# Optimization experiments

Hardware: AMD Instinct MI355X
Metric: run time of the kernel (lower is better)

The kernel has to match this reference:

```python
import jax, jax.numpy as jnp
import numpy as np

IT = 3  # BP iterations
ROWS, N = 144, 576  # H dims: wman_N0576_R34 -> 144 checks, 576 vars
ROW_DEG = 6  # check-node degree


def _make_H():
    rng = np.random.default_rng(0)
    H = np.zeros((ROWS, N), np.float32)
    for i in range(ROWS):
        cols = rng.choice(N, size=ROW_DEG, replace=False)
        H[i, cols] = 1.0
    return jnp.asarray(H)


def _quantize(x, eta, qk):
    # 4-level soft quantization: softmax over -(x-qk)^2/(2 eta^2)
    logits = -(x[..., None] - qk) ** 2 / (2.0 * eta ** 2 + 1e-12)
    w = jax.nn.softmax(logits, axis=-1)
    return jnp.sum(w * qk, axis=-1)


def setup_inputs() -> dict:
    key = jax.random.key(0)
    k1, = jax.random.split(key, 1)
    batch = 512
    r = jax.random.normal(k1, (batch, N), dtype=jnp.float32)
    H = _make_H()
    alpha = jnp.ones((IT,), jnp.float32) * 0.7
    beta = jnp.ones((IT,), jnp.float32) * 0.05
    eta = jnp.ones((IT,), jnp.float32) * 0.7
    qk = jnp.linspace(-4.0, 4.0, 4).astype(jnp.float32)
    return {"r": r, "H": H, "alpha": alpha, "beta": beta, "eta": eta, "qk": qk}


def reference(r, H, alpha, beta, eta, qk):
    B, n = r.shape
    Hmask = H == 1
    node_idx = jnp.arange(n)[None, None, :]
    M = H[None] * r[:, None, :]          # (B, ROWS, N)
    E = jnp.zeros_like(M)
    for t in range(IT):
        # --- check-to-variable (min-sum with masked top-2) ---
        masked_abs = jnp.where(Hmask, jnp.abs(M), jnp.inf)
        neg_top, idx = jax.lax.top_k(-masked_abs, 2)  # two smallest
        min1 = -neg_top[..., 0:1]
        min2 = -neg_top[..., 1:2]
        idx1 = idx[..., 0:1]
        E_abs = jnp.where(node_idx == idx1, min2, min1)
        signs = jnp.sign(M)
        valid_signs = jnp.where(Hmask, signs, 1.0)
        row_sign_prod = jnp.prod(valid_signs, axis=2, keepdims=True)
        E_sign = row_sign_prod * valid_signs
        E = alpha[t] * E_sign * jnp.maximum(0.0, E_abs - beta[t])
        E = E * H
        E = _quantize(E, eta[t], qk)
        # --- variable-to-check update ---
        sum_E = jnp.sum(E, axis=1, keepdims=True)
        M = (r[:, None, :] + sum_E - E) * H[None]
        M = _quantize(M, eta[t], qk)
    return r + jnp.sum(E, axis=1)
```

## Files before the change

kernel.cpp:

```cpp
#include <hip/hip_runtime.h>
#include <math.h>

#define IT 3
#define ROWS 144
#define NCOLS 576
#define ROW_DEG 6

__device__ __forceinline__ float quantize4(float x, float inv2e,
                                           float q0, float q1, float q2, float q3) {
    float d0 = x - q0, d1 = x - q1, d2 = x - q2, d3 = x - q3;
    float l0 = -d0 * d0 * inv2e;
    float l1 = -d1 * d1 * inv2e;
    float l2 = -d2 * d2 * inv2e;
    float l3 = -d3 * d3 * inv2e;
    float mx = fmaxf(fmaxf(l0, l1), fmaxf(l2, l3));
    float w0 = __expf(l0 - mx), w1 = __expf(l1 - mx);
    float w2 = __expf(l2 - mx), w3 = __expf(l3 - mx);
    float s = w0 + w1 + w2 + w3;
    return (w0 * q0 + w1 * q1 + w2 * q2 + w3 * q3) / s;
}

__device__ __forceinline__ float signf(float x) {
    return (x > 0.0f) ? 1.0f : ((x < 0.0f) ? -1.0f : 0.0f);
}

__global__ __launch_bounds__(64) void extract_cols_kernel(
    const float* __restrict__ H, int* __restrict__ cols)
{
    const int row  = blockIdx.x;
    const int lane = threadIdx.x;
    int base = 0;
    for (int i = 0; i < NCOLS / 64; ++i) {
        int col = i * 64 + lane;
        bool nz = H[row * NCOLS + col] != 0.0f;
        unsigned long long mask = __ballot(nz);
        if (nz) {
            int rank = base + __popcll(mask & ((1ull << lane) - 1ull));
            if (rank < ROW_DEG) cols[row * ROW_DEG + rank] = col;
        }
        base += __popcll(mask);
    }
}

__global__ __launch_bounds__(192) void decode_kernel(
    const float* __restrict__ r, const int* __restrict__ cols,
    const float* __restrict__ alpha, const float* __restrict__ beta,
    const float* __restrict__ eta, const float* __restrict__ qk,
    float* __restrict__ out)
{
    __shared__ float s_r[NCOLS];
    __shared__ float s_sumE[NCOLS];

    const int b = blockIdx.x;
    const float* rb = r + (size_t)b * NCOLS;
    for (int j = threadIdx.x; j < NCOLS; j += blockDim.x) s_r[j] = rb[j];

    const float q0 = qk[0], q1 = qk[1], q2 = qk[2], q3 = qk[3];
    float al[IT], be[IT], i2e[IT];
    for (int t = 0; t < IT; ++t) {
        al[t] = alpha[t];
        be[t] = beta[t];
        float et = eta[t];
        i2e[t] = 1.0f / (2.0f * et * et + 1e-12f);
    }

    const int row = threadIdx.x;
    const bool active = row < ROWS;

    int   c[ROW_DEG];
    float m[ROW_DEG];
    float E[ROW_DEG];

    __syncthreads();
    if (active) {
        for (int e = 0; e < ROW_DEG; ++e) {
            c[e] = cols[row * ROW_DEG + e];
            m[e] = s_r[c[e]];
        }
    }

    for (int t = 0; t < IT; ++t) {
        const float inv2e = i2e[t];

        __syncthreads();
        for (int j = threadIdx.x; j < NCOLS; j += blockDim.x) s_sumE[j] = 0.0f;
        __syncthreads();

        if (active) {
            float min1 = INFINITY, min2 = INFINITY;
            int idx = -1;
            float sp = 1.0f;
            for (int e = 0; e < ROW_DEG; ++e) {
                float a = fabsf(m[e]);
                sp *= signf(m[e]);
                if (a < min1) { min2 = min1; min1 = a; idx = e; }
                else if (a < min2) { min2 = a; }
            }
            for (int e = 0; e < ROW_DEG; ++e) {
                float eabs = (e == idx) ? min2 : min1;
                float v = al[t] * sp * signf(m[e]) * fmaxf(0.0f, eabs - be[t]);
                v = quantize4(v, inv2e, q0, q1, q2, q3);
                E[e] = v;
                atomicAdd(&s_sumE[c[e]], v);
            }
        }
        __syncthreads();

        if (t < IT - 1 && active) {
            for (int e = 0; e < ROW_DEG; ++e) {
                float v = s_r[c[e]] + s_sumE[c[e]] - E[e];
                m[e] = quantize4(v, inv2e, q0, q1, q2, q3);
            }
        }
    }

    float* ob = out + (size_t)b * NCOLS;
    for (int j = threadIdx.x; j < NCOLS; j += blockDim.x) ob[j] = s_r[j] + s_sumE[j];
}

extern "C" void kernel_launch(void* const* d_in, const int* in_sizes, int n_in,
                              void* d_out, int out_size, void* d_ws, size_t ws_size,
                              hipStream_t stream) {
    const float* r     = (const float*)d_in[0];
    const float* H     = (const float*)d_in[1];
    const float* alpha = (const float*)d_in[2];
    const float* beta  = (const float*)d_in[3];
    const float* eta   = (const float*)d_in[4];
    const float* qk    = (const float*)d_in[5];
    float* out = (float*)d_out;

    int* cols = (int*)d_ws;
    const int batch = in_sizes[0] / NCOLS;

    hipLaunchKernelGGL(extract_cols_kernel, dim3(ROWS), dim3(64), 0, stream,
                       H, cols);
    hipLaunchKernelGGL(decode_kernel, dim3(batch), dim3(192), 0, stream,
                       r, cols, alpha, beta, eta, qk, out);
}
```

Baseline: 80.72 us.

## Fuse column extraction into decoder and use single-exp quantizer

Removes the separate column-extraction kernel: each block now scans H itself and keeps the column indices in shared memory. The 4-level softmax quantizer is rewritten as one exp of a scaled input plus two cubic polynomials in that exponential, with precomputed per-iteration constants. This assumes the quantization levels are evenly spaced and clamps the exponent. Row/output copies are vectorized to float4. Every block now redundantly reads all of H, which adds L2 traffic in exchange for dropping one launch.

```diff
diff --git a/kernel.cpp b/kernel.cpp
--- a/kernel.cpp
+++ b/kernel.cpp
@@ -5,66 +5,77 @@
 #define ROWS 144
 #define NCOLS 576
 #define ROW_DEG 6
+#define NTHREADS 192
+#define NWAVES 3
 
-__device__ __forceinline__ float quantize4(float x, float inv2e,
-                                           float q0, float q1, float q2, float q3) {
-    float d0 = x - q0, d1 = x - q1, d2 = x - q2, d3 = x - q3;
-    float l0 = -d0 * d0 * inv2e;
-    float l1 = -d1 * d1 * inv2e;
-    float l2 = -d2 * d2 * inv2e;
-    float l3 = -d3 * d3 * inv2e;
-    float mx = fmaxf(fmaxf(l0, l1), fmaxf(l2, l3));
-    float w0 = __expf(l0 - mx), w1 = __expf(l1 - mx);
-    float w2 = __expf(l2 - mx), w3 = __expf(l3 - mx);
-    float s = w0 + w1 + w2 + w3;
-    return (w0 * q0 + w1 * q1 + w2 * q2 + w3 * q3) / s;
+__device__ __forceinline__ float quantize1(float x, float S,
+                                           float K0, float K1, float K2, float K3,
+                                           float KQ0, float KQ1, float KQ2, float KQ3) {
+    float s = fminf(fmaxf(x * S, -30.0f), 30.0f);
+    float B = __expf(s);
+    float den = ((K3 * B + K2) * B + K1) * B + K0;
+    float num = ((KQ3 * B + KQ2) * B + KQ1) * B + KQ0;
+    return num * __builtin_amdgcn_rcpf(den);
 }
 
 __device__ __forceinline__ float signf(float x) {
     return (x > 0.0f) ? 1.0f : ((x < 0.0f) ? -1.0f : 0.0f);
 }
 
-__global__ __launch_bounds__(64) void extract_cols_kernel(
-    const float* __restrict__ H, int* __restrict__ cols)
-{
-    const int row  = blockIdx.x;
-    const int lane = threadIdx.x;
-    int base = 0;
-    for (int i = 0; i < NCOLS / 64; ++i) {
-        int col = i * 64 + lane;
-        bool nz = H[row * NCOLS + col] != 0.0f;
-        unsigned long long mask = __ballot(nz);
-        if (nz) {
-            int rank = base + __popcll(mask & ((1ull << lane) - 1ull));
-            if (rank < ROW_DEG) cols[row * ROW_DEG + rank] = col;
-        }
-        base += __popcll(mask);
-    }
-}
-
-__global__ __launch_bounds__(192) void decode_kernel(
-    const float* __restrict__ r, const int* __restrict__ cols,
+__global__ __launch_bounds__(NTHREADS) void decode_kernel(
+    const float* __restrict__ r, const float* __restrict__ H,
     const float* __restrict__ alpha, const float* __restrict__ beta,
     const float* __restrict__ eta, const float* __restrict__ qk,
     float* __restrict__ out)
 {
-    __shared__ float s_r[NCOLS];
-    __shared__ float s_sumE[NCOLS];
+    __shared__ __align__(16) float s_r[NCOLS];
+    __shared__ __align__(16) float s_sumE[NCOLS];
+    __shared__ int s_cols[ROWS * ROW_DEG];
 
-    const int b = blockIdx.x;
-    const float* rb = r + (size_t)b * NCOLS;
-    for (int j = threadIdx.x; j < NCOLS; j += blockDim.x) s_r[j] = rb[j];
+    const int b   = blockIdx.x;
+    const int tid = threadIdx.x;
+
+    const float4* rb4 = reinterpret_cast<const float4*>(r + (size_t)b * NCOLS);
+    float4* s_r4 = reinterpret_cast<float4*>(s_r);
+    for (int j = tid; j < NCOLS / 4; j += NTHREADS) s_r4[j] = rb4[j];
+
+    {
+        const int wv = tid >> 6, lane = tid & 63;
+        for (int rr = wv; rr < ROWS; rr += NWAVES) {
+            float hv[9];
+            #pragma unroll
+            for (int i = 0; i < 9; ++i) hv[i] = H[rr * NCOLS + i * 64 + lane];
+            int base = 0;
+            #pragma unroll
+            for (int i = 0; i < 9; ++i) {
+                bool nz = hv[i] != 0.0f;
+                unsigned long long mk = __ballot(nz);
+                if (nz) {
+                    int rank = base + __popcll(mk & ((1ull << lane) - 1ull));
+                    if (rank < ROW_DEG) s_cols[rr * ROW_DEG + rank] = i * 64 + lane;
+                }
+                base += __popcll(mk);
+            }
+        }
+    }
 
     const float q0 = qk[0], q1 = qk[1], q2 = qk[2], q3 = qk[3];
-    float al[IT], be[IT], i2e[IT];
+    const float dq = (q3 - q0) * (1.0f / 3.0f);
+    float al[IT], be[IT], sc[IT];
+    float k0[IT], k1[IT], k2[IT], k3[IT];
+    #pragma unroll
     for (int t = 0; t < IT; ++t) {
         al[t] = alpha[t];
         be[t] = beta[t];
-        float et = eta[t];
-        i2e[t] = 1.0f / (2.0f * et * et + 1e-12f);
+        float inv2e = 1.0f / (2.0f * eta[t] * eta[t] + 1e-12f);
+        sc[t] = 2.0f * dq * inv2e;
+        k0[t] = __expf(-q0 * q0 * inv2e);
+        k1[t] = __expf(-q1 * q1 * inv2e);
+        k2[t] = __expf(-q2 * q2 * inv2e);
+        k3[t] = __expf(-q3 * q3 * inv2e);
     }
 
-    const int row = threadIdx.x;
+    const int row = tid;
     const bool active = row < ROWS;
 
     int   c[ROW_DEG];
@@ -73,33 +84,39 @@
 
     __syncthreads();
     if (active) {
+        #pragma unroll
         for (int e = 0; e < ROW_DEG; ++e) {
-            c[e] = cols[row * ROW_DEG + e];
+            c[e] = s_cols[row * ROW_DEG + e];
             m[e] = s_r[c[e]];
         }
     }
 
+    #pragma unroll
     for (int t = 0; t < IT; ++t) {
-        const float inv2e = i2e[t];
+        __syncthreads();
+        for (int j = tid; j < NCOLS; j += NTHREADS) s_sumE[j] = 0.0f;
+        __syncthreads();
 
-        __syncthreads();
-        for (int j = threadIdx.x; j < NCOLS; j += blockDim.x) s_sumE[j] = 0.0f;
-        __syncthreads();
+        const float A = al[t], Bt = be[t], S = sc[t];
+        const float K0 = k0[t], K1 = k1[t], K2 = k2[t], K3 = k3[t];
+        const float KQ0 = K0 * q0, KQ1 = K1 * q1, KQ2 = K2 * q2, KQ3 = K3 * q3;
 
         if (active) {
             float min1 = INFINITY, min2 = INFINITY;
             int idx = -1;
             float sp = 1.0f;
+            #pragma unroll
             for (int e = 0; e < ROW_DEG; ++e) {
                 float a = fabsf(m[e]);
                 sp *= signf(m[e]);
                 if (a < min1) { min2 = min1; min1 = a; idx = e; }
                 else if (a < min2) { min2 = a; }
             }
+            #pragma unroll
             for (int e = 0; e < ROW_DEG; ++e) {
                 float eabs = (e == idx) ? min2 : min1;
-                float v = al[t] * sp * signf(m[e]) * fmaxf(0.0f, eabs - be[t]);
-                v = quantize4(v, inv2e, q0, q1, q2, q3);
+                float v = A * sp * signf(m[e]) * fmaxf(0.0f, eabs - Bt);
+                v = quantize1(v, S, K0, K1, K2, K3, KQ0, KQ1, KQ2, KQ3);
                 E[e] = v;
                 atomicAdd(&s_sumE[c[e]], v);
             }
@@ -107,15 +124,23 @@
         __syncthreads();
 
         if (t < IT - 1 && active) {
+            #pragma unroll
             for (int e = 0; e < ROW_DEG; ++e) {
                 float v = s_r[c[e]] + s_sumE[c[e]] - E[e];
-                m[e] = quantize4(v, inv2e, q0, q1, q2, q3);
+                m[e] = quantize1(v, S, K0, K1, K2, K3, KQ0, KQ1, KQ2, KQ3);
             }
         }
     }
 
-    float* ob = out + (size_t)b * NCOLS;
-    for (int j = threadIdx.x; j < NCOLS; j += blockDim.x) ob[j] = s_r[j] + s_sumE[j];
+    float4* ob4 = reinterpret_cast<float4*>(out + (size_t)b * NCOLS);
+    float4* s_s4 = reinterpret_cast<float4*>(s_sumE);
+    for (int j = tid; j < NCOLS / 4; j += NTHREADS) {
+        float4 rv = s_r4[j], sv = s_s4[j];
+        float4 o;
+        o.x = rv.x + sv.x; o.y = rv.y + sv.y;
+        o.z = rv.z + sv.z; o.w = rv.w + sv.w;
+        ob4[j] = o;
+    }
 }
 
 extern "C" void kernel_launch(void* const* d_in, const int* in_sizes, int n_in,
@@ -129,11 +154,10 @@
     const float* qk    = (const float*)d_in[5];
     float* out = (float*)d_out;
 
-    int* cols = (int*)d_ws;
     const int batch = in_sizes[0] / NCOLS;
 
-    hipLaunchKernelGGL(extract_cols_kernel, dim3(ROWS), dim3(64), 0, stream,
-                       H, cols);
-    hipLaunchKernelGGL(decode_kernel, dim3(batch), dim3(192), 0, stream,
-                       r, cols, alpha, beta, eta, qk, out);
+    (void)d_ws; (void)ws_size;
+
+    hipLaunchKernelGGL(decode_kernel, dim3(batch), dim3(NTHREADS), 0, stream,
+                       r, H, alpha, beta, eta, qk, out);
 }
```

Result: slower. 104.0 us (+28.9%).
